# Performance work log

Hardware: AMD Instinct MI355X
Metric: run time of the kernel (lower is better)

Reference implementation:

```python
import jax, jax.numpy as jnp
import numpy as np

HEADS = 4
OUT_CH = 64
NEG_SLOPE = 0.2  # PyG GATConv default negative_slope


def setup_inputs() -> dict:
    key = jax.random.key(0)
    k1, k2, k3, k4, k5, k6 = jax.random.split(key, 6)
    N, E, IN_CH = 50000, 800000, 128
    x = jax.random.normal(k1, (N, IN_CH), dtype=jnp.float32)
    edge_index = jax.random.randint(k2, (2, E), 0, N, dtype=jnp.int64)
    # Learned parameters (glorot-style init)
    s_w = (6.0 / (IN_CH + HEADS * OUT_CH)) ** 0.5
    W = jax.random.uniform(k3, (IN_CH, HEADS * OUT_CH), minval=-s_w, maxval=s_w, dtype=jnp.float32)
    s_a = (6.0 / (1 + OUT_CH)) ** 0.5
    att_src = jax.random.uniform(k4, (HEADS, OUT_CH), minval=-s_a, maxval=s_a, dtype=jnp.float32)
    att_dst = jax.random.uniform(k5, (HEADS, OUT_CH), minval=-s_a, maxval=s_a, dtype=jnp.float32)
    bias = jnp.zeros((HEADS * OUT_CH,), dtype=jnp.float32)
    return {"x": x, "W": W, "att_src": att_src, "att_dst": att_dst, "bias": bias, "edge_index": edge_index}


def reference(x, W, att_src, att_dst, bias, edge_index):
    # Faithful GATConv (PyG defaults: add_self_loops=True, concat=True, eval mode => no dropout)
    N = x.shape[0]
    loops = jnp.arange(N, dtype=edge_index.dtype)
    src = jnp.concatenate([edge_index[0], loops])  # message source j
    dst = jnp.concatenate([edge_index[1], loops])  # message target i

    xp = (x @ W).reshape(N, HEADS, OUT_CH)          # [N, H, C]
    a_src = jnp.einsum('nhc,hc->nh', xp, att_src)   # [N, H]
    a_dst = jnp.einsum('nhc,hc->nh', xp, att_dst)   # [N, H]

    alpha = jax.nn.leaky_relu(a_src[src] + a_dst[dst], NEG_SLOPE)  # [E', H]
    # segment softmax over incoming edges of each target node
    amax = jax.ops.segment_max(alpha, dst, num_segments=N)
    ex = jnp.exp(alpha - jax.lax.stop_gradient(amax)[dst])
    denom = jax.ops.segment_sum(ex, dst, num_segments=N)
    coef = ex / denom[dst]                           # [E', H]

    msg = xp[src] * coef[:, :, None]                 # [E', H, C]
    out = jax.ops.segment_sum(msg, dst, num_segments=N)  # [N, H, C]
    return out.reshape(N, HEADS * OUT_CH) + bias
```

## Files before the change

kernel.cpp:

```cpp
#include <hip/hip_runtime.h>

#define HEADS 4
#define OUTC 64
#define INC 128
#define HC 256
#define NEG 0.2f

typedef __attribute__((ext_vector_type(8))) short bf16x8;
typedef __attribute__((ext_vector_type(4))) float f32x4;

static __device__ __forceinline__ float bf2f(unsigned short u){
  unsigned int x = ((unsigned int)u) << 16;
  return __uint_as_float(x);
}
static __device__ __forceinline__ unsigned short f2bf(float f){
  unsigned int x = __float_as_uint(f);
  unsigned int lsb = (x >> 16) & 1u;
  x += 0x7fffu + lsb;
  return (unsigned short)(x >> 16);
}
static __device__ __forceinline__ void split8(float4 a, float4 b, bf16x8& hi, bf16x8& lo){
  float v[8] = {a.x, a.y, a.z, a.w, b.x, b.y, b.z, b.w};
  #pragma unroll
  for (int i = 0; i < 8; ++i){
    unsigned short h = f2bf(v[i]);
    hi[i] = (short)h;
    lo[i] = (short)f2bf(v[i] - bf2f(h));
  }
}

__global__ void k_conv_e_hist(const int* __restrict__ ei,
                              int* __restrict__ srcc, int* __restrict__ dstc,
                              int* __restrict__ pos, int* __restrict__ deg, int E){
  int e = blockIdx.x * 256 + threadIdx.x;
  bool valid = (e < E);
  int ee = valid ? e : 0;
  int hiw = ei[2 * ee + 1];
  bool hz = valid ? (hiw == 0) : true;
  unsigned long long mask = __ballot(hz);
  bool i64 = (mask == ~0ULL);
  int s, d;
  if (i64){ s = ei[2 * ee]; d = ei[2 * (size_t)E + 2 * ee]; }
  else    { s = ei[ee];     d = ei[(size_t)E + ee]; }
  if (valid){
    srcc[e] = s; dstc[e] = d;
    pos[e] = atomicAdd(&deg[d], 1);
  }
}

__global__ void k_split_w(const float* __restrict__ W, unsigned short* __restrict__ Wthi,
                          unsigned short* __restrict__ Wtlo){
  int t = blockIdx.x * 256 + threadIdx.x;
  int k = t >> 8, n = t & 255;
  float v = W[t];
  unsigned short hi = f2bf(v);
  Wthi[n * INC + k] = hi;
  Wtlo[n * INC + k] = f2bf(v - bf2f(hi));
}

__global__ __launch_bounds__(256) void k_gemm_fused(const float* __restrict__ X,
    const unsigned short* __restrict__ Wthi, const unsigned short* __restrict__ Wtlo,
    const float* __restrict__ att_src, const float* __restrict__ att_dst,
    unsigned short* __restrict__ XPh, float* __restrict__ a_src, float* __restrict__ a_dst,
    int N){
  int w = threadIdx.x >> 6, lane = threadIdx.x & 63;
  int m0 = blockIdx.x * 64;
  int quad = lane >> 4;
  int l15 = lane & 15;
  int colg[4];
  #pragma unroll
  for (int t = 0; t < 4; ++t) colg[t] = w * 64 + t * 16 + l15;

  bool rv[4]; int rowr[4];
  #pragma unroll
  for (int rt = 0; rt < 4; ++rt){
    rv[rt] = (m0 + rt * 16) < N;
    rowr[rt] = rv[rt] ? (m0 + rt * 16 + l15) : 0;
  }

  f32x4 acc[4][4];
  #pragma unroll
  for (int rt = 0; rt < 4; ++rt)
    #pragma unroll
    for (int t = 0; t < 4; ++t) acc[rt][t] = (f32x4){0.f, 0.f, 0.f, 0.f};

  #pragma unroll
  for (int kk = 0; kk < 4; ++kk){
    float4 va[4], vb[4];
    #pragma unroll
    for (int rt = 0; rt < 4; ++rt){
      const float* xr = X + (size_t)rowr[rt] * INC + kk * 32 + quad * 8;
      va[rt] = *(const float4*)xr;
      vb[rt] = *(const float4*)(xr + 4);
    }
    bf16x8 bh[4], bl[4];
    #pragma unroll
    for (int t = 0; t < 4; ++t){
      size_t bo = (size_t)colg[t] * INC + kk * 32 + quad * 8;
      bh[t] = *(const bf16x8*)(Wthi + bo);
      bl[t] = *(const bf16x8*)(Wtlo + bo);
    }
    bf16x8 ah[4], al[4];
    #pragma unroll
    for (int rt = 0; rt < 4; ++rt) split8(va[rt], vb[rt], ah[rt], al[rt]);
    #pragma unroll
    for (int rt = 0; rt < 4; ++rt){
      #pragma unroll
      for (int t = 0; t < 4; ++t){
        acc[rt][t] = __builtin_amdgcn_mfma_f32_16x16x32_bf16(ah[rt], bh[t], acc[rt][t], 0, 0, 0);
        acc[rt][t] = __builtin_amdgcn_mfma_f32_16x16x32_bf16(ah[rt], bl[t], acc[rt][t], 0, 0, 0);
        acc[rt][t] = __builtin_amdgcn_mfma_f32_16x16x32_bf16(al[rt], bh[t], acc[rt][t], 0, 0, 0);
      }
    }
  }

  #pragma unroll
  for (int rt = 0; rt < 4; ++rt){
    if (!rv[rt]) continue;
    #pragma unroll
    for (int t = 0; t < 4; ++t){
      #pragma unroll
      for (int r = 0; r < 4; ++r){
        XPh[(size_t)(m0 + rt * 16 + quad * 4 + r) * HC + colg[t]] = f2bf(acc[rt][t][r]);
      }
    }
  }

  float as[4], ad[4];
  #pragma unroll
  for (int t = 0; t < 4; ++t){
    as[t] = att_src[colg[t]];
    ad[t] = att_dst[colg[t]];
  }
  #pragma unroll
  for (int rt = 0; rt < 4; ++rt){
    if (!rv[rt]) continue;
    float ps[4], pd[4];
    #pragma unroll
    for (int r = 0; r < 4; ++r){
      ps[r] = acc[rt][0][r] * as[0] + acc[rt][1][r] * as[1]
            + acc[rt][2][r] * as[2] + acc[rt][3][r] * as[3];
      pd[r] = acc[rt][0][r] * ad[0] + acc[rt][1][r] * ad[1]
            + acc[rt][2][r] * ad[2] + acc[rt][3][r] * ad[3];
    }
    #pragma unroll
    for (int msk = 1; msk < 16; msk <<= 1){
      #pragma unroll
      for (int r = 0; r < 4; ++r){
        ps[r] += __shfl_xor(ps[r], msk, 64);
        pd[r] += __shfl_xor(pd[r], msk, 64);
      }
    }
    if (l15 == 0){
      #pragma unroll
      for (int r = 0; r < 4; ++r){
        int n = m0 + rt * 16 + quad * 4 + r;
        a_src[n * HEADS + w] = ps[r];
        a_dst[n * HEADS + w] = pd[r];
      }
    }
  }
}

__global__ __launch_bounds__(256) void k_scan1(const int* __restrict__ deg,
                                               int* __restrict__ out,
                                               int* __restrict__ bsum, int N){
  __shared__ int tsum[256];
  int t = threadIdx.x;
  int base = blockIdx.x * 1024 + t * 4;
  int v[4]; int s = 0;
  #pragma unroll
  for (int k = 0; k < 4; ++k){ int i = base + k; v[k] = (i < N) ? deg[i] : 0; s += v[k]; }
  tsum[t] = s;
  __syncthreads();
  for (int off = 1; off < 256; off <<= 1){
    int x = (t >= off) ? tsum[t - off] : 0;
    __syncthreads();
    tsum[t] += x;
    __syncthreads();
  }
  int excl = tsum[t] - s;
  if (t == 255) bsum[blockIdx.x] = tsum[255];
  int run = excl;
  #pragma unroll
  for (int k = 0; k < 4; ++k){ int i = base + k; if (i < N) out[i] = run; run += v[k]; }
}

__global__ __launch_bounds__(256) void k_scan23(int* __restrict__ rowstart,
                                                const int* __restrict__ bsum,
                                                int N, int E){
  int lane = threadIdx.x & 63;
  int partial = 0;
  for (int i = lane; i < blockIdx.x; i += 64) partial += bsum[i];
  #pragma unroll
  for (int msk = 32; msk; msk >>= 1) partial += __shfl_xor(partial, msk, 64);
  int base = blockIdx.x * 1024 + threadIdx.x * 4;
  #pragma unroll
  for (int k = 0; k < 4; ++k){ int i = base + k; if (i < N) rowstart[i] += partial; }
  if (blockIdx.x == 0 && threadIdx.x == 0) rowstart[N] = E;
}

__global__ void k_scatter(const int* __restrict__ srcc, const int* __restrict__ dstc,
                          const int* __restrict__ pos, const int* __restrict__ rowstart,
                          int* __restrict__ csr, int E){
  int e = blockIdx.x * 256 + threadIdx.x;
  if (e < E){
    int d = dstc[e];
    csr[rowstart[d] + pos[e]] = srcc[e];
  }
}

__global__ __launch_bounds__(256) void k_fused(const unsigned short* __restrict__ XPh,
    const float* __restrict__ a_src, const float* __restrict__ a_dst,
    const int* __restrict__ rowstart, const int* __restrict__ csr,
    const float* __restrict__ bias, float* __restrict__ out, int N){
  __shared__ float sh[4][64][4];
  int w = threadIdx.x >> 6, lane = threadIdx.x & 63;
  int n = blockIdx.x * 4 + w;
  bool alive = (n < N);
  if (!alive) n = 0;
  int r0 = rowstart[n], r1 = rowstart[n + 1];
  int deg = r1 - r0;
  int total = deg + 1;
  int h = lane >> 4;
  float4 ad4 = *(const float4*)&a_dst[n * HEADS];
  bool fast = (total <= 64);
  int jv = n;
  float msel = 0.f, inv_sel = 0.f;

  if (fast){
    if (lane < deg) jv = csr[r0 + lane];
    float l0 = -1e30f, l1 = -1e30f, l2 = -1e30f, l3 = -1e30f;
    if (lane < total){
      float4 a4 = *(const float4*)&a_src[jv * HEADS];
      l0 = a4.x + ad4.x; l0 = (l0 > 0.f) ? l0 : NEG * l0;
      l1 = a4.y + ad4.y; l1 = (l1 > 0.f) ? l1 : NEG * l1;
      l2 = a4.z + ad4.z; l2 = (l2 > 0.f) ? l2 : NEG * l2;
      l3 = a4.w + ad4.w; l3 = (l3 > 0.f) ? l3 : NEG * l3;
    }
    float p0 = __expf(l0), p1 = __expf(l1), p2 = __expf(l2), p3 = __expf(l3);
    float s0 = p0, s1 = p1, s2 = p2, s3 = p3;
    #pragma unroll
    for (int msk = 32; msk; msk >>= 1){
      s0 += __shfl_xor(s0, msk, 64);
      s1 += __shfl_xor(s1, msk, 64);
      s2 += __shfl_xor(s2, msk, 64);
      s3 += __shfl_xor(s3, msk, 64);
    }
    if (lane < total){
      sh[w][lane][0] = p0 / s0;
      sh[w][lane][1] = p1 / s1;
      sh[w][lane][2] = p2 / s2;
      sh[w][lane][3] = p3 / s3;
    }
  } else {
    float m[4] = {-1e30f, -1e30f, -1e30f, -1e30f};
    float s[4] = {0.f, 0.f, 0.f, 0.f};
    float adArr[4] = {ad4.x, ad4.y, ad4.z, ad4.w};
    for (int e = lane; e < total; e += 64){
      int j = (e < deg) ? csr[r0 + e] : n;
      float4 a4 = *(const float4*)&a_src[j * HEADS];
      float aa[4] = {a4.x, a4.y, a4.z, a4.w};
      #pragma unroll
      for (int hh = 0; hh < 4; ++hh){
        float l = aa[hh] + adArr[hh];
        l = (l > 0.f) ? l : NEG * l;
        if (l > m[hh]){ s[hh] = s[hh] * __expf(m[hh] - l) + 1.f; m[hh] = l; }
        else            s[hh] += __expf(l - m[hh]);
      }
    }
    #pragma unroll
    for (int hh = 0; hh < 4; ++hh){
      float mm = m[hh], ss = s[hh];
      #pragma unroll
      for (int msk = 32; msk; msk >>= 1){
        float m2 = __shfl_xor(mm, msk, 64);
        float s2 = __shfl_xor(ss, msk, 64);
        float M = fmaxf(mm, m2);
        float ns = 0.f;
        if (mm > -1e29f) ns += ss * __expf(mm - M);
        if (m2 > -1e29f) ns += s2 * __expf(m2 - M);
        mm = M; ss = ns;
      }
      m[hh] = mm; s[hh] = ss;
    }
    msel    = (h == 0) ? m[0] : (h == 1) ? m[1] : (h == 2) ? m[2] : m[3];
    inv_sel = 1.f / ((h == 0) ? s[0] : (h == 1) ? s[1] : (h == 2) ? s[2] : s[3]);
  }

  __syncthreads();

  float a0 = 0.f, a1 = 0.f, a2 = 0.f, a3 = 0.f;
  const unsigned short* xb = XPh + lane * 4;
  if (fast){
    int e = 0;
    for (; e + 8 <= total; e += 8){
      int jj[8]; float cf[8]; ushort4 xv[8];
      #pragma unroll
      for (int q = 0; q < 8; ++q){
        jj[q] = __builtin_amdgcn_readlane(jv, e + q);
        cf[q] = sh[w][e + q][h];
      }
      #pragma unroll
      for (int q = 0; q < 8; ++q) xv[q] = *(const ushort4*)(xb + (size_t)jj[q] * HC);
      #pragma unroll
      for (int q = 0; q < 8; ++q){
        a0 += cf[q] * bf2f(xv[q].x); a1 += cf[q] * bf2f(xv[q].y);
        a2 += cf[q] * bf2f(xv[q].z); a3 += cf[q] * bf2f(xv[q].w);
      }
    }
    for (; e < total; ++e){
      int j = __builtin_amdgcn_readlane(jv, e);
      float c = sh[w][e][h];
      ushort4 xv = *(const ushort4*)(xb + (size_t)j * HC);
      a0 += c * bf2f(xv.x); a1 += c * bf2f(xv.y); a2 += c * bf2f(xv.z); a3 += c * bf2f(xv.w);
    }
  } else {
    float adh = (h == 0) ? ad4.x : (h == 1) ? ad4.y : (h == 2) ? ad4.z : ad4.w;
    for (int e = 0; e < total; ++e){
      int j = (e < deg) ? csr[r0 + e] : n;
      float4 a4 = *(const float4*)&a_src[j * HEADS];
      float ah = (h == 0) ? a4.x : (h == 1) ? a4.y : (h == 2) ? a4.z : a4.w;
      float l = ah + adh;
      l = (l > 0.f) ? l : NEG * l;
      float c = __expf(l - msel) * inv_sel;
      ushort4 xv = *(const ushort4*)(xb + (size_t)j * HC);
      a0 += c * bf2f(xv.x); a1 += c * bf2f(xv.y); a2 += c * bf2f(xv.z); a3 += c * bf2f(xv.w);
    }
  }
  if (alive){
    float4 b4 = *(const float4*)&bias[lane * 4];
    float4 r; r.x = a0 + b4.x; r.y = a1 + b4.y; r.z = a2 + b4.z; r.w = a3 + b4.w;
    *(float4*)&out[(size_t)n * HC + lane * 4] = r;
  }
}

extern "C" void kernel_launch(void* const* d_in, const int* in_sizes, int n_in,
                              void* d_out, int out_size, void* d_ws, size_t ws_size,
                              hipStream_t stream){
  const float* x       = (const float*)d_in[0];
  const float* W       = (const float*)d_in[1];
  const float* att_src = (const float*)d_in[2];
  const float* att_dst = (const float*)d_in[3];
  const float* bias    = (const float*)d_in[4];
  const int*   ei      = (const int*)d_in[5];
  int N = in_sizes[0] / INC;
  int E = in_sizes[5] / 2;

  char* p = (char*)d_ws;
  auto alloc = [&](size_t bytes)->char*{
    char* r = p; p += (bytes + 255) & ~(size_t)255; return r;
  };
  unsigned short* Wthi = (unsigned short*)alloc((size_t)INC * HC * 2);
  unsigned short* Wtlo = (unsigned short*)alloc((size_t)INC * HC * 2);
  unsigned short* XPh  = (unsigned short*)alloc((size_t)N * HC * 2);
  float* aSrc          = (float*)alloc((size_t)N * HEADS * 4);
  float* aDst          = (float*)alloc((size_t)N * HEADS * 4);
  int* deg             = (int*)alloc((size_t)N * 4);
  int* rowstart        = (int*)alloc(((size_t)N + 1) * 4);
  int* srcc            = (int*)alloc((size_t)E * 4);
  int* dstc            = (int*)alloc((size_t)E * 4);
  int* pos             = (int*)alloc((size_t)E * 4);
  int* csr             = (int*)alloc((size_t)E * 4);
  int* bsum            = (int*)alloc(256 * 4);

  hipMemsetAsync(deg, 0, (size_t)N * 4, stream);
  k_conv_e_hist<<<(E + 255) / 256, 256, 0, stream>>>(ei, srcc, dstc, pos, deg, E);

  k_split_w<<<(INC * HC) / 256, 256, 0, stream>>>(W, Wthi, Wtlo);
  k_gemm_fused<<<(N + 63) / 64, 256, 0, stream>>>(x, Wthi, Wtlo, att_src, att_dst,
                                                  XPh, aSrc, aDst, N);

  int nb = (N + 1023) / 1024;
  k_scan1<<<nb, 256, 0, stream>>>(deg, rowstart, bsum, N);
  k_scan23<<<nb, 256, 0, stream>>>(rowstart, bsum, N, E);
  k_scatter<<<(E + 255) / 256, 256, 0, stream>>>(srcc, dstc, pos, rowstart, csr, E);

  k_fused<<<(N + 3) / 4, 256, 0, stream>>>(XPh, aSrc, aDst, rowstart, csr, bias,
                                           (float*)d_out, N);
}
```

Before: 249.4 us.

## Retile GEMM per-wave row strip and split aggregation across two edge halves

The projection GEMM now gives each wave a 16-row strip across all 256 columns, so X is loaded and split into bf16 hi/lo once per row instead of once per column group. The attention-logit reduction is reworked to match the new layout. The aggregation kernel has each half-wave handle alternate edges with 16-byte gathers of 8 bf16 values, then combines the halves with a cross-lane shuffle. The output is written with nontemporal stores. Together these aim to widen memory transactions and double the number of gathers in flight, at the cost of more registers in the GEMM (16 accumulators) and extra shuffles.

New measurement: 282.3 us. 1.13x slower.

```diff
diff --git a/kernel.cpp b/kernel.cpp
--- a/kernel.cpp
+++ b/kernel.cpp
@@ -12,6 +12,12 @@
 static __device__ __forceinline__ float bf2f(unsigned short u){
   unsigned int x = ((unsigned int)u) << 16;
   return __uint_as_float(x);
+}
+static __device__ __forceinline__ float bflo(unsigned int u){
+  return __uint_as_float(u << 16);
+}
+static __device__ __forceinline__ float bfhi(unsigned int u){
+  return __uint_as_float(u & 0xffff0000u);
 }
 static __device__ __forceinline__ unsigned short f2bf(float f){
   unsigned int x = __float_as_uint(f);
@@ -64,100 +70,79 @@
     unsigned short* __restrict__ XPh, float* __restrict__ a_src, float* __restrict__ a_dst,
     int N){
   int w = threadIdx.x >> 6, lane = threadIdx.x & 63;
-  int m0 = blockIdx.x * 64;
-  int quad = lane >> 4;
-  int l15 = lane & 15;
-  int colg[4];
-  #pragma unroll
-  for (int t = 0; t < 4; ++t) colg[t] = w * 64 + t * 16 + l15;
-
-  bool rv[4]; int rowr[4];
-  #pragma unroll
-  for (int rt = 0; rt < 4; ++rt){
-    rv[rt] = (m0 + rt * 16) < N;
-    rowr[rt] = rv[rt] ? (m0 + rt * 16 + l15) : 0;
-  }
-
-  f32x4 acc[4][4];
-  #pragma unroll
-  for (int rt = 0; rt < 4; ++rt)
-    #pragma unroll
-    for (int t = 0; t < 4; ++t) acc[rt][t] = (f32x4){0.f, 0.f, 0.f, 0.f};
+  int quad = lane >> 4, l15 = lane & 15;
+  int rt = blockIdx.x * 4 + w;
+  int row0 = rt * 16;
+  if (row0 >= N) return;
+  int row = row0 + l15;
+
+  f32x4 acc[16];
+  #pragma unroll
+  for (int t = 0; t < 16; ++t) acc[t] = (f32x4){0.f, 0.f, 0.f, 0.f};
 
   #pragma unroll
   for (int kk = 0; kk < 4; ++kk){
-    float4 va[4], vb[4];
-    #pragma unroll
-    for (int rt = 0; rt < 4; ++rt){
-      const float* xr = X + (size_t)rowr[rt] * INC + kk * 32 + quad * 8;
-      va[rt] = *(const float4*)xr;
-      vb[rt] = *(const float4*)(xr + 4);
-    }
-    bf16x8 bh[4], bl[4];
-    #pragma unroll
-    for (int t = 0; t < 4; ++t){
-      size_t bo = (size_t)colg[t] * INC + kk * 32 + quad * 8;
-      bh[t] = *(const bf16x8*)(Wthi + bo);
-      bl[t] = *(const bf16x8*)(Wtlo + bo);
-    }
-    bf16x8 ah[4], al[4];
-    #pragma unroll
-    for (int rt = 0; rt < 4; ++rt) split8(va[rt], vb[rt], ah[rt], al[rt]);
-    #pragma unroll
-    for (int rt = 0; rt < 4; ++rt){
-      #pragma unroll
-      for (int t = 0; t < 4; ++t){
-        acc[rt][t] = __builtin_amdgcn_mfma_f32_16x16x32_bf16(ah[rt], bh[t], acc[rt][t], 0, 0, 0);
-        acc[rt][t] = __builtin_amdgcn_mfma_f32_16x16x32_bf16(ah[rt], bl[t], acc[rt][t], 0, 0, 0);
-        acc[rt][t] = __builtin_amdgcn_mfma_f32_16x16x32_bf16(al[rt], bh[t], acc[rt][t], 0, 0, 0);
-      }
-    }
-  }
-
-  #pragma unroll
-  for (int rt = 0; rt < 4; ++rt){
-    if (!rv[rt]) continue;
-    #pragma unroll
-    for (int t = 0; t < 4; ++t){
-      #pragma unroll
-      for (int r = 0; r < 4; ++r){
-        XPh[(size_t)(m0 + rt * 16 + quad * 4 + r) * HC + colg[t]] = f2bf(acc[rt][t][r]);
-      }
-    }
-  }
-
-  float as[4], ad[4];
-  #pragma unroll
-  for (int t = 0; t < 4; ++t){
-    as[t] = att_src[colg[t]];
-    ad[t] = att_dst[colg[t]];
-  }
-  #pragma unroll
-  for (int rt = 0; rt < 4; ++rt){
-    if (!rv[rt]) continue;
-    float ps[4], pd[4];
+    const float* xr = X + (size_t)row * INC + kk * 32 + quad * 8;
+    float4 va = *(const float4*)xr;
+    float4 vb = *(const float4*)(xr + 4);
+    bf16x8 ah, al;
+    split8(va, vb, ah, al);
+    #pragma unroll
+    for (int tg = 0; tg < 4; ++tg){
+      bf16x8 bh[4], bl[4];
+      #pragma unroll
+      for (int q = 0; q < 4; ++q){
+        size_t bo = (size_t)((tg * 4 + q) * 16 + l15) * INC + kk * 32 + quad * 8;
+        bh[q] = *(const bf16x8*)(Wthi + bo);
+        bl[q] = *(const bf16x8*)(Wtlo + bo);
+      }
+      #pragma unroll
+      for (int q = 0; q < 4; ++q){
+        int t = tg * 4 + q;
+        acc[t] = __builtin_amdgcn_mfma_f32_16x16x32_bf16(ah, bh[q], acc[t], 0, 0, 0);
+        acc[t] = __builtin_amdgcn_mfma_f32_16x16x32_bf16(ah, bl[q], acc[t], 0, 0, 0);
+        acc[t] = __builtin_amdgcn_mfma_f32_16x16x32_bf16(al, bh[q], acc[t], 0, 0, 0);
+      }
+    }
+  }
+
+  #pragma unroll
+  for (int t = 0; t < 16; ++t){
     #pragma unroll
     for (int r = 0; r < 4; ++r){
-      ps[r] = acc[rt][0][r] * as[0] + acc[rt][1][r] * as[1]
-            + acc[rt][2][r] * as[2] + acc[rt][3][r] * as[3];
-      pd[r] = acc[rt][0][r] * ad[0] + acc[rt][1][r] * ad[1]
-            + acc[rt][2][r] * ad[2] + acc[rt][3][r] * ad[3];
-    }
-    #pragma unroll
-    for (int msk = 1; msk < 16; msk <<= 1){
-      #pragma unroll
-      for (int r = 0; r < 4; ++r){
-        ps[r] += __shfl_xor(ps[r], msk, 64);
-        pd[r] += __shfl_xor(pd[r], msk, 64);
-      }
-    }
-    if (l15 == 0){
-      #pragma unroll
-      for (int r = 0; r < 4; ++r){
-        int n = m0 + rt * 16 + quad * 4 + r;
-        a_src[n * HEADS + w] = ps[r];
-        a_dst[n * HEADS + w] = pd[r];
-      }
+      XPh[(size_t)(row0 + quad * 4 + r) * HC + t * 16 + l15] = f2bf(acc[t][r]);
+    }
+  }
+
+  float as_[16], ad_[16];
+  #pragma unroll
+  for (int t = 0; t < 16; ++t){
+    as_[t] = att_src[t * 16 + l15];
+    ad_[t] = att_dst[t * 16 + l15];
+  }
+  #pragma unroll
+  for (int r = 0; r < 4; ++r){
+    float psel = 0.f, pdel = 0.f;
+    #pragma unroll
+    for (int hh = 0; hh < 4; ++hh){
+      float sv = 0.f, dv = 0.f;
+      #pragma unroll
+      for (int q = 0; q < 4; ++q){
+        int t = hh * 4 + q;
+        sv += acc[t][r] * as_[t];
+        dv += acc[t][r] * ad_[t];
+      }
+      #pragma unroll
+      for (int msk = 1; msk < 16; msk <<= 1){
+        sv += __shfl_xor(sv, msk, 64);
+        dv += __shfl_xor(dv, msk, 64);
+      }
+      if (l15 == hh){ psel = sv; pdel = dv; }
+    }
+    int nrow = row0 + quad * 4 + r;
+    if (l15 < 4){
+      a_src[nrow * HEADS + l15] = psel;
+      a_dst[nrow * HEADS + l15] = pdel;
     }
   }
 }
@@ -222,11 +207,11 @@
   int r0 = rowstart[n], r1 = rowstart[n + 1];
   int deg = r1 - r0;
   int total = deg + 1;
-  int h = lane >> 4;
   float4 ad4 = *(const float4*)&a_dst[n * HEADS];
   bool fast = (total <= 64);
   int jv = n;
-  float msel = 0.f, inv_sel = 0.f;
+  float mH0 = 0.f, mH1 = 0.f, mH2 = 0.f, mH3 = 0.f;
+  float iH0 = 0.f, iH1 = 0.f, iH2 = 0.f, iH3 = 0.f;
 
   if (fast){
     if (lane < deg) jv = csr[r0 + lane];
@@ -248,10 +233,8 @@
       s3 += __shfl_xor(s3, msk, 64);
     }
     if (lane < total){
-      sh[w][lane][0] = p0 / s0;
-      sh[w][lane][1] = p1 / s1;
-      sh[w][lane][2] = p2 / s2;
-      sh[w][lane][3] = p3 / s3;
+      float4 cv; cv.x = p0 / s0; cv.y = p1 / s1; cv.z = p2 / s2; cv.w = p3 / s3;
+      *(float4*)&sh[w][lane][0] = cv;
     }
   } else {
     float m[4] = {-1e30f, -1e30f, -1e30f, -1e30f};
@@ -284,54 +267,79 @@
       }
       m[hh] = mm; s[hh] = ss;
     }
-    msel    = (h == 0) ? m[0] : (h == 1) ? m[1] : (h == 2) ? m[2] : m[3];
-    inv_sel = 1.f / ((h == 0) ? s[0] : (h == 1) ? s[1] : (h == 2) ? s[2] : s[3]);
+    mH0 = m[0]; mH1 = m[1]; mH2 = m[2]; mH3 = m[3];
+    iH0 = 1.f / s[0]; iH1 = 1.f / s[1]; iH2 = 1.f / s[2]; iH3 = 1.f / s[3];
   }
 
   __syncthreads();
 
-  float a0 = 0.f, a1 = 0.f, a2 = 0.f, a3 = 0.f;
-  const unsigned short* xb = XPh + lane * 4;
+  int half = lane >> 5, l32 = lane & 31;
+  int hh = l32 >> 3;
+  const unsigned short* xb = XPh + l32 * 8;
+  float a0 = 0.f, a1 = 0.f, a2 = 0.f, a3 = 0.f, a4_ = 0.f, a5 = 0.f, a6 = 0.f, a7 = 0.f;
+
   if (fast){
-    int e = 0;
-    for (; e + 8 <= total; e += 8){
-      int jj[8]; float cf[8]; ushort4 xv[8];
+    for (int e = 0; e < total; e += 16){
+      int jj[8]; float cf[8];
       #pragma unroll
       for (int q = 0; q < 8; ++q){
-        jj[q] = __builtin_amdgcn_readlane(jv, e + q);
-        cf[q] = sh[w][e + q][h];
-      }
-      #pragma unroll
-      for (int q = 0; q < 8; ++q) xv[q] = *(const ushort4*)(xb + (size_t)jj[q] * HC);
+        int s0i = e + 2 * q, s1i = s0i + 1;
+        int c0 = (s0i < total) ? s0i : (total - 1);
+        int c1 = (s1i < total) ? s1i : (total - 1);
+        int j0 = __builtin_amdgcn_readlane(jv, c0);
+        int j1 = __builtin_amdgcn_readlane(jv, c1);
+        jj[q] = half ? j1 : j0;
+        int sl = s0i + half;
+        int slc = (sl < total) ? sl : 0;
+        cf[q] = (sl < total) ? sh[w][slc][hh] : 0.f;
+      }
+      uint4 xv[8];
+      #pragma unroll
+      for (int q = 0; q < 8; ++q) xv[q] = *(const uint4*)(xb + (size_t)jj[q] * HC);
       #pragma unroll
       for (int q = 0; q < 8; ++q){
-        a0 += cf[q] * bf2f(xv[q].x); a1 += cf[q] * bf2f(xv[q].y);
-        a2 += cf[q] * bf2f(xv[q].z); a3 += cf[q] * bf2f(xv[q].w);
-      }
-    }
-    for (; e < total; ++e){
-      int j = __builtin_amdgcn_readlane(jv, e);
-      float c = sh[w][e][h];
-      ushort4 xv = *(const ushort4*)(xb + (size_t)j * HC);
-      a0 += c * bf2f(xv.x); a1 += c * bf2f(xv.y); a2 += c * bf2f(xv.z); a3 += c * bf2f(xv.w);
+        float c = cf[q];
+        a0  += c * bflo(xv[q].x); a1 += c * bfhi(xv[q].x);
+        a2  += c * bflo(xv[q].y); a3 += c * bfhi(xv[q].y);
+        a4_ += c * bflo(xv[q].z); a5 += c * bfhi(xv[q].z);
+        a6  += c * bflo(xv[q].w); a7 += c * bfhi(xv[q].w);
+      }
     }
   } else {
-    float adh = (h == 0) ? ad4.x : (h == 1) ? ad4.y : (h == 2) ? ad4.z : ad4.w;
-    for (int e = 0; e < total; ++e){
-      int j = (e < deg) ? csr[r0 + e] : n;
-      float4 a4 = *(const float4*)&a_src[j * HEADS];
-      float ah = (h == 0) ? a4.x : (h == 1) ? a4.y : (h == 2) ? a4.z : a4.w;
-      float l = ah + adh;
+    float adh = (hh == 0) ? ad4.x : (hh == 1) ? ad4.y : (hh == 2) ? ad4.z : ad4.w;
+    float mh  = (hh == 0) ? mH0 : (hh == 1) ? mH1 : (hh == 2) ? mH2 : mH3;
+    float ih  = (hh == 0) ? iH0 : (hh == 1) ? iH1 : (hh == 2) ? iH2 : iH3;
+    for (int e = 0; e < total; e += 2){
+      int eh = e + half;
+      bool has = (eh < total);
+      int ec = has ? eh : (total - 1);
+      int j = (ec < deg) ? csr[r0 + ec] : n;
+      float4 s4 = *(const float4*)&a_src[j * HEADS];
+      float ahv = (hh == 0) ? s4.x : (hh == 1) ? s4.y : (hh == 2) ? s4.z : s4.w;
+      float l = ahv + adh;
       l = (l > 0.f) ? l : NEG * l;
-      float c = __expf(l - msel) * inv_sel;
-      ushort4 xv = *(const ushort4*)(xb + (size_t)j * HC);
-      a0 += c * bf2f(xv.x); a1 += c * bf2f(xv.y); a2 += c * bf2f(xv.z); a3 += c * bf2f(xv.w);
-    }
-  }
+      float c = has ? (__expf(l - mh) * ih) : 0.f;
+      uint4 xv = *(const uint4*)(xb + (size_t)j * HC);
+      a0  += c * bflo(xv.x); a1 += c * bfhi(xv.x);
+      a2  += c * bflo(xv.y); a3 += c * bfhi(xv.y);
+      a4_ += c * bflo(xv.z); a5 += c * bfhi(xv.z);
+      a6  += c * bflo(xv.w); a7 += c * bfhi(xv.w);
+    }
+  }
+
+  a0  += __shfl_xor(a0, 32, 64);  a1 += __shfl_xor(a1, 32, 64);
+  a2  += __shfl_xor(a2, 32, 64);  a3 += __shfl_xor(a3, 32, 64);
+  a4_ += __shfl_xor(a4_, 32, 64); a5 += __shfl_xor(a5, 32, 64);
+  a6  += __shfl_xor(a6, 32, 64);  a7 += __shfl_xor(a7, 32, 64);
+
   if (alive){
-    float4 b4 = *(const float4*)&bias[lane * 4];
-    float4 r; r.x = a0 + b4.x; r.y = a1 + b4.y; r.z = a2 + b4.z; r.w = a3 + b4.w;
-    *(float4*)&out[(size_t)n * HC + lane * 4] = r;
+    float4 b4 = *(const float4*)&bias[l32 * 8 + half * 4];
+    f32x4 r;
+    r[0] = (half ? a4_ : a0) + b4.x;
+    r[1] = (half ? a5  : a1) + b4.y;
+    r[2] = (half ? a6  : a2) + b4.z;
+    r[3] = (half ? a7  : a3) + b4.w;
+    __builtin_nontemporal_store(r, (f32x4*)&out[(size_t)n * HC + l32 * 8 + half * 4]);
   }
 }
 
```

## Split fused aggregation into coefficient and per-head gather kernels with head-major XP

Applied to the files above, without the earlier changes.

Stores the projected features head-major (separate N x 64 planes per head) and splits the aggregation kernel in two. The first kernel computes the softmax coefficients per edge into a buffer. The second runs one grid slice per head, where each wave handles a node and processes four edges at a time, with 16 lanes per edge reading 128 bytes. The intent is a smaller per-head working set for gathers (12.8MB per plane) that fits in cache better, plus more parallelism. The cost is an extra kernel launch and writing and re-reading 4E coefficients, with the edge-list temporaries aliased into the coefficient buffer.

New measurement: 364.4 us. 1.46x slower.

```diff
diff --git a/kernel.cpp b/kernel.cpp
--- a/kernel.cpp
+++ b/kernel.cpp
@@ -12,6 +12,12 @@
 static __device__ __forceinline__ float bf2f(unsigned short u){
   unsigned int x = ((unsigned int)u) << 16;
   return __uint_as_float(x);
+}
+static __device__ __forceinline__ float bflo(unsigned int u){
+  return __uint_as_float(u << 16);
+}
+static __device__ __forceinline__ float bfhi(unsigned int u){
+  return __uint_as_float(u & 0xffff0000u);
 }
 static __device__ __forceinline__ unsigned short f2bf(float f){
   unsigned int x = __float_as_uint(f);
@@ -61,8 +67,8 @@
 __global__ __launch_bounds__(256) void k_gemm_fused(const float* __restrict__ X,
     const unsigned short* __restrict__ Wthi, const unsigned short* __restrict__ Wtlo,
     const float* __restrict__ att_src, const float* __restrict__ att_dst,
-    unsigned short* __restrict__ XPh, float* __restrict__ a_src, float* __restrict__ a_dst,
-    int N){
+    unsigned short* __restrict__ XPh , float* __restrict__ a_src,
+    float* __restrict__ a_dst, int N){
   int w = threadIdx.x >> 6, lane = threadIdx.x & 63;
   int m0 = blockIdx.x * 64;
   int quad = lane >> 4;
@@ -121,7 +127,8 @@
     for (int t = 0; t < 4; ++t){
       #pragma unroll
       for (int r = 0; r < 4; ++r){
-        XPh[(size_t)(m0 + rt * 16 + quad * 4 + r) * HC + colg[t]] = f2bf(acc[rt][t][r]);
+        XPh[((size_t)w * N + (m0 + rt * 16 + quad * 4 + r)) * OUTC + t * 16 + l15]
+          = f2bf(acc[rt][t][r]);
       }
     }
   }
@@ -210,25 +217,20 @@
   }
 }
 
-__global__ __launch_bounds__(256) void k_fused(const unsigned short* __restrict__ XPh,
-    const float* __restrict__ a_src, const float* __restrict__ a_dst,
-    const int* __restrict__ rowstart, const int* __restrict__ csr,
-    const float* __restrict__ bias, float* __restrict__ out, int N){
-  __shared__ float sh[4][64][4];
+__global__ __launch_bounds__(256) void k_coef(const float* __restrict__ a_src,
+    const float* __restrict__ a_dst, const int* __restrict__ rowstart,
+    const int* __restrict__ csr, float* __restrict__ coefc ,
+    float* __restrict__ selfc , int N, int E){
   int w = threadIdx.x >> 6, lane = threadIdx.x & 63;
   int n = blockIdx.x * 4 + w;
-  bool alive = (n < N);
-  if (!alive) n = 0;
+  if (n >= N) return;
   int r0 = rowstart[n], r1 = rowstart[n + 1];
   int deg = r1 - r0;
   int total = deg + 1;
-  int h = lane >> 4;
   float4 ad4 = *(const float4*)&a_dst[n * HEADS];
-  bool fast = (total <= 64);
-  int jv = n;
-  float msel = 0.f, inv_sel = 0.f;
-
-  if (fast){
+
+  if (total <= 64){
+    int jv = n;
     if (lane < deg) jv = csr[r0 + lane];
     float l0 = -1e30f, l1 = -1e30f, l2 = -1e30f, l3 = -1e30f;
     if (lane < total){
@@ -247,11 +249,14 @@
       s2 += __shfl_xor(s2, msk, 64);
       s3 += __shfl_xor(s3, msk, 64);
     }
-    if (lane < total){
-      sh[w][lane][0] = p0 / s0;
-      sh[w][lane][1] = p1 / s1;
-      sh[w][lane][2] = p2 / s2;
-      sh[w][lane][3] = p3 / s3;
+    if (lane < deg){
+      coefc[0 * (size_t)E + r0 + lane] = p0 / s0;
+      coefc[1 * (size_t)E + r0 + lane] = p1 / s1;
+      coefc[2 * (size_t)E + r0 + lane] = p2 / s2;
+      coefc[3 * (size_t)E + r0 + lane] = p3 / s3;
+    } else if (lane == deg){
+      f32x4 sv; sv[0] = p0 / s0; sv[1] = p1 / s1; sv[2] = p2 / s2; sv[3] = p3 / s3;
+      *(f32x4*)&selfc[n * HEADS] = sv;
     }
   } else {
     float m[4] = {-1e30f, -1e30f, -1e30f, -1e30f};
@@ -284,54 +289,61 @@
       }
       m[hh] = mm; s[hh] = ss;
     }
-    msel    = (h == 0) ? m[0] : (h == 1) ? m[1] : (h == 2) ? m[2] : m[3];
-    inv_sel = 1.f / ((h == 0) ? s[0] : (h == 1) ? s[1] : (h == 2) ? s[2] : s[3]);
-  }
-
-  __syncthreads();
-
-  float a0 = 0.f, a1 = 0.f, a2 = 0.f, a3 = 0.f;
-  const unsigned short* xb = XPh + lane * 4;
-  if (fast){
-    int e = 0;
-    for (; e + 8 <= total; e += 8){
-      int jj[8]; float cf[8]; ushort4 xv[8];
-      #pragma unroll
-      for (int q = 0; q < 8; ++q){
-        jj[q] = __builtin_amdgcn_readlane(jv, e + q);
-        cf[q] = sh[w][e + q][h];
-      }
-      #pragma unroll
-      for (int q = 0; q < 8; ++q) xv[q] = *(const ushort4*)(xb + (size_t)jj[q] * HC);
-      #pragma unroll
-      for (int q = 0; q < 8; ++q){
-        a0 += cf[q] * bf2f(xv[q].x); a1 += cf[q] * bf2f(xv[q].y);
-        a2 += cf[q] * bf2f(xv[q].z); a3 += cf[q] * bf2f(xv[q].w);
-      }
-    }
-    for (; e < total; ++e){
-      int j = __builtin_amdgcn_readlane(jv, e);
-      float c = sh[w][e][h];
-      ushort4 xv = *(const ushort4*)(xb + (size_t)j * HC);
-      a0 += c * bf2f(xv.x); a1 += c * bf2f(xv.y); a2 += c * bf2f(xv.z); a3 += c * bf2f(xv.w);
-    }
-  } else {
-    float adh = (h == 0) ? ad4.x : (h == 1) ? ad4.y : (h == 2) ? ad4.z : ad4.w;
-    for (int e = 0; e < total; ++e){
+    float inv[4] = {1.f / s[0], 1.f / s[1], 1.f / s[2], 1.f / s[3]};
+    for (int e = lane; e < total; e += 64){
       int j = (e < deg) ? csr[r0 + e] : n;
       float4 a4 = *(const float4*)&a_src[j * HEADS];
-      float ah = (h == 0) ? a4.x : (h == 1) ? a4.y : (h == 2) ? a4.z : a4.w;
-      float l = ah + adh;
-      l = (l > 0.f) ? l : NEG * l;
-      float c = __expf(l - msel) * inv_sel;
-      ushort4 xv = *(const ushort4*)(xb + (size_t)j * HC);
-      a0 += c * bf2f(xv.x); a1 += c * bf2f(xv.y); a2 += c * bf2f(xv.z); a3 += c * bf2f(xv.w);
-    }
-  }
-  if (alive){
-    float4 b4 = *(const float4*)&bias[lane * 4];
-    float4 r; r.x = a0 + b4.x; r.y = a1 + b4.y; r.z = a2 + b4.z; r.w = a3 + b4.w;
-    *(float4*)&out[(size_t)n * HC + lane * 4] = r;
+      float aa[4] = {a4.x, a4.y, a4.z, a4.w};
+      #pragma unroll
+      for (int hh = 0; hh < 4; ++hh){
+        float l = aa[hh] + adArr[hh];
+        l = (l > 0.f) ? l : NEG * l;
+        float c = __expf(l - m[hh]) * inv[hh];
+        if (e < deg) coefc[(size_t)hh * E + r0 + e] = c;
+        else         selfc[n * HEADS + hh] = c;
+      }
+    }
+  }
+}
+
+__global__ __launch_bounds__(256) void k_gather(const unsigned short* __restrict__ XPh,
+    const float* __restrict__ coefc, const float* __restrict__ selfc,
+    const int* __restrict__ rowstart, const int* __restrict__ csr,
+    const float* __restrict__ bias, float* __restrict__ out, int N, int E){
+  int w = threadIdx.x >> 6, lane = threadIdx.x & 63;
+  int h = blockIdx.y;
+  int n = blockIdx.x * 4 + w;
+  if (n >= N) return;
+  int q = lane >> 4, l16 = lane & 15;
+  int r0 = rowstart[n], deg = rowstart[n + 1] - r0;
+  int total = deg + 1;
+  const unsigned short* xh = XPh + (size_t)h * N * OUTC + l16 * 4;
+  const float* ch = coefc + (size_t)h * E + r0;
+  float cself = selfc[n * HEADS + h];
+
+  float a0 = 0.f, a1 = 0.f, a2 = 0.f, a3 = 0.f;
+  for (int e0 = 0; e0 < total; e0 += 4){
+    int e = e0 + q;
+    bool v = (e < total);
+    int ec = v ? e : 0;
+    bool isedge = (ec < deg);
+    int j = isedge ? __builtin_nontemporal_load(&csr[r0 + ec]) : n;
+    float c = 0.f;
+    if (v) c = isedge ? __builtin_nontemporal_load(&ch[ec]) : cself;
+    uint2 xv = *(const uint2*)(xh + (size_t)j * OUTC);
+    a0 += c * bflo(xv.x); a1 += c * bfhi(xv.x);
+    a2 += c * bflo(xv.y); a3 += c * bfhi(xv.y);
+  }
+  a0 += __shfl_xor(a0, 16, 64); a0 += __shfl_xor(a0, 32, 64);
+  a1 += __shfl_xor(a1, 16, 64); a1 += __shfl_xor(a1, 32, 64);
+  a2 += __shfl_xor(a2, 16, 64); a2 += __shfl_xor(a2, 32, 64);
+  a3 += __shfl_xor(a3, 16, 64); a3 += __shfl_xor(a3, 32, 64);
+
+  if (q == 0){
+    float4 b4 = *(const float4*)&bias[h * OUTC + l16 * 4];
+    f32x4 r;
+    r[0] = a0 + b4.x; r[1] = a1 + b4.y; r[2] = a2 + b4.z; r[3] = a3 + b4.w;
+    __builtin_nontemporal_store(r, (f32x4*)&out[(size_t)n * HC + h * OUTC + l16 * 4]);
   }
 }
 
@@ -358,10 +370,12 @@
   float* aDst          = (float*)alloc((size_t)N * HEADS * 4);
   int* deg             = (int*)alloc((size_t)N * 4);
   int* rowstart        = (int*)alloc(((size_t)N + 1) * 4);
-  int* srcc            = (int*)alloc((size_t)E * 4);
-  int* dstc            = (int*)alloc((size_t)E * 4);
-  int* pos             = (int*)alloc((size_t)E * 4);
   int* csr             = (int*)alloc((size_t)E * 4);
+  float* coefc         = (float*)alloc((size_t)HEADS * E * 4);
+  int* srcc            = (int*)coefc;
+  int* dstc            = srcc + E;
+  int* pos             = dstc + E;
+  float* selfc         = (float*)alloc((size_t)N * HEADS * 4);
   int* bsum            = (int*)alloc(256 * 4);
 
   hipMemsetAsync(deg, 0, (size_t)N * 4, stream);
@@ -376,6 +390,9 @@
   k_scan23<<<nb, 256, 0, stream>>>(rowstart, bsum, N, E);
   k_scatter<<<(E + 255) / 256, 256, 0, stream>>>(srcc, dstc, pos, rowstart, csr, E);
 
-  k_fused<<<(N + 3) / 4, 256, 0, stream>>>(XPh, aSrc, aDst, rowstart, csr, bias,
-                                           (float*)d_out, N);
-}
+  k_coef<<<(N + 3) / 4, 256, 0, stream>>>(aSrc, aDst, rowstart, csr, coefc, selfc, N, E);
+
+  dim3 ggrid((N + 3) / 4, HEADS);
+  k_gather<<<ggrid, 256, 0, stream>>>(XPh, coefc, selfc, rowstart, csr, bias,
+                                      (float*)d_out, N, E);
+}
```
